# Kernel tuning notes

Hardware: AMD Instinct MI355X
Metric: run time of the kernel (lower is better)

Reference implementation:

```python
import jax, jax.numpy as jnp
import numpy as np

B, N, E = 1024, 4096, 16384
MAX_COL_W, ROW_W = 4, 8


def setup_inputs() -> dict:
    key = jax.random.key(0)
    k1, k2, k3, k4, k5 = jax.random.split(key, 5)
    return {
        "channelLLR": jax.random.normal(k1, (B, N), dtype=jnp.float32),
        "e2oLLR": jax.random.normal(k2, (B, E), dtype=jnp.float32),
        "maxColWeight": MAX_COL_W,
        "edgeToVar": jax.random.randint(k3, (B, N, MAX_COL_W), 0, E, dtype=jnp.int32),
        "edgeToVarMask": jnp.ones((B, N, MAX_COL_W), dtype=jnp.float32),
        "oddToEven": jax.random.randint(k4, (B, E), 0, N, dtype=jnp.int32),
        "edgeToChk": jax.random.randint(k5, (B, E, ROW_W - 1), 0, E, dtype=jnp.int32),
        "rowWeight": ROW_W,
        "alpha": jnp.ones((1,), dtype=jnp.float32),
    }


def reference(channelLLR, e2oLLR, maxColWeight, edgeToVar, edgeToVarMask,
              oddToEven, edgeToChk, rowWeight, alpha):
    b = channelLLR.shape[0]
    # variable-node update: gather incoming edge messages, mask, sum
    msgToVars = jnp.take_along_axis(e2oLLR, edgeToVar.reshape(b, -1), axis=1)
    msgToVars = msgToVars.reshape(b, -1, maxColWeight) * edgeToVarMask  # [B,N,colW]
    llr = channelLLR + jnp.sum(msgToVars, axis=2)                      # [B,N]
    # extrinsic variable-to-check message per edge
    llr = jnp.take_along_axis(llr, oddToEven, axis=1) - e2oLLR         # [B,E]
    # check-node min-sum update over rowWeight-1 peer edges
    msgToChecks = jnp.take_along_axis(llr, edgeToChk.reshape(b, -1), axis=1)
    msgToChecks = msgToChecks.reshape(b, -1, rowWeight - 1)            # [B,E,rowW-1]
    mn = jnp.min(jnp.abs(msgToChecks), axis=2)                         # [B,E]
    sign = jnp.prod(jnp.sign(msgToChecks), axis=2)                     # [B,E]
    e2o = sign * (mn * alpha[0])                                       # [B,E]
    # marginalized posterior LLR per variable node
    out = jnp.take_along_axis(e2o, edgeToVar.reshape(b, -1), axis=1)
    out = out.reshape(b, -1, maxColWeight) * edgeToVarMask
    out = channelLLR + jnp.sum(out, axis=2)                            # [B,N]
    return (out, e2o)
```

## Files before the change

kernel.cpp:

```cpp
#include <hip/hip_runtime.h>

#define BB   1024
#define NN   4096
#define EE   16384
#define COLW 4
#define ROWW1 7
#define TPB  1024
#define NWAVE (TPB / 64)
#define GRP_DW (64 * ROWW1)
#define SCR_DW (NWAVE * GRP_DW)

__global__ __launch_bounds__(TPB) void msl_fused_kernel(
    const float* __restrict__ channelLLR,
    const float* __restrict__ e2oLLR,
    const int*   __restrict__ edgeToVar,
    const float* __restrict__ edgeToVarMask,
    const int*   __restrict__ oddToEven,
    const int*   __restrict__ edgeToChk,
    const float* __restrict__ alpha,
    float*       __restrict__ out,
    float*       __restrict__ e2o_out)
{
    __shared__ __align__(16) float scr_lds[2 * SCR_DW];
    __shared__ __align__(16) float edge_lds[EE];
    const int b    = blockIdx.x;
    const int tid  = threadIdx.x;
    const int wave = tid >> 6;
    const int lane = tid & 63;
    const float alph = alpha[0];

    {
        const float4* __restrict__ src = reinterpret_cast<const float4*>(e2oLLR + (size_t)b * EE);
        float4* dst = reinterpret_cast<float4*>(edge_lds);
        #pragma unroll
        for (int k = 0; k < EE / 4 / TPB; ++k) {
            int i = tid + k * TPB;
            dst[i] = src[i];
        }
    }
    __syncthreads();

    int4   idxreg[NN / TPB];
    float4 mreg[NN / TPB];
    {
        const int4*   __restrict__ ev4 = reinterpret_cast<const int4*>(edgeToVar + (size_t)b * NN * COLW);
        const float4* __restrict__ mk4 = reinterpret_cast<const float4*>(edgeToVarMask + (size_t)b * NN * COLW);
        const float*  __restrict__ chrow = channelLLR + (size_t)b * NN;
        #pragma unroll
        for (int k = 0; k < NN / TPB; ++k) {
            int n = tid + k * TPB;
            int4  idx = ev4[n];
            float4 m  = mk4[n];
            float acc = chrow[n];
            acc += edge_lds[idx.x] * m.x;
            acc += edge_lds[idx.y] * m.y;
            acc += edge_lds[idx.z] * m.z;
            acc += edge_lds[idx.w] * m.w;
            scr_lds[n] = acc;
            idxreg[k] = idx; mreg[k] = m;
        }
    }
    __syncthreads();

    {
        const int* __restrict__ o2erow = oddToEven + (size_t)b * EE;
        #pragma unroll 8
        for (int k = 0; k < EE / TPB; ++k) {
            int e = tid + k * TPB;
            int o = o2erow[e];
            float v = scr_lds[o] - edge_lds[e];
            edge_lds[e] = v;
        }
    }
    __syncthreads();

    float e2oreg[EE / TPB];
    {
        const int* __restrict__ ecrow = edgeToChk + (size_t)b * (size_t)EE * ROWW1;
        float* __restrict__ e2orow = e2o_out + (size_t)b * EE;
        int idx[ROWW1];
        {
            const int* __restrict__ p = ecrow + (size_t)wave * GRP_DW + lane;
            #pragma unroll
            for (int j = 0; j < ROWW1; ++j) idx[j] = p[64 * j];
        }
        #pragma unroll
        for (int it = 0; it < EE / TPB; ++it) {
            const int g = it * NWAVE + wave;
            float* __restrict__ scratch = scr_lds + (it & 1) * SCR_DW + wave * GRP_DW;
            #pragma unroll
            for (int j = 0; j < ROWW1; ++j) scratch[lane + 64 * j] = edge_lds[idx[j]];
            if (it + 1 < EE / TPB) {
                const int* __restrict__ p = ecrow + (size_t)(g + NWAVE) * GRP_DW + lane;
                #pragma unroll
                for (int j = 0; j < ROWW1; ++j) idx[j] = p[64 * j];
            }
            __builtin_amdgcn_wave_barrier();
            asm volatile("s_waitcnt lgkmcnt(0)" ::: "memory");
            __builtin_amdgcn_wave_barrier();
            float mn = 3.0e38f;
            unsigned sgn = 0u;
            const float* __restrict__ sb = scratch + lane * ROWW1;
            #pragma unroll
            for (int j = 0; j < ROWW1; ++j) {
                float u = sb[j];
                sgn ^= __float_as_uint(u);
                mn = fminf(mn, fabsf(u));
            }
            float val = mn * alph;
            float r = __uint_as_float(__float_as_uint(val) ^ (sgn & 0x80000000u));
            e2oreg[it] = r;
            e2orow[64 * g + lane] = r;
        }
    }
    __syncthreads();

    #pragma unroll
    for (int k = 0; k < EE / TPB; ++k) {
        edge_lds[tid + k * TPB] = e2oreg[k];
    }
    __syncthreads();

    {
        float* __restrict__ outrow = out + (size_t)b * NN;
        const float* __restrict__ chrow = channelLLR + (size_t)b * NN;
        #pragma unroll
        for (int k = 0; k < NN / TPB; ++k) {
            int n = tid + k * TPB;
            int4  idx = idxreg[k];
            float4 m  = mreg[k];
            float acc = chrow[n];
            acc += edge_lds[idx.x] * m.x;
            acc += edge_lds[idx.y] * m.y;
            acc += edge_lds[idx.z] * m.z;
            acc += edge_lds[idx.w] * m.w;
            outrow[n] = acc;
        }
    }
}

extern "C" void kernel_launch(void* const* d_in, const int* in_sizes, int n_in,
                              void* d_out, int out_size, void* d_ws, size_t ws_size,
                              hipStream_t stream) {
    const float* channelLLR    = (const float*)d_in[0];
    const float* e2oLLR        = (const float*)d_in[1];
    const int*   edgeToVar     = (const int*)d_in[3];
    const float* edgeToVarMask = (const float*)d_in[4];
    const int*   oddToEven     = (const int*)d_in[5];
    const int*   edgeToChk     = (const int*)d_in[6];
    const float* alpha         = (const float*)d_in[8];

    float* out     = (float*)d_out;
    float* e2o_out = (float*)d_out + (size_t)BB * NN;

    msl_fused_kernel<<<BB, TPB, 0, stream>>>(
        channelLLR, e2oLLR, edgeToVar, edgeToVarMask,
        oddToEven, edgeToChk, alpha, out, e2o_out);
}
```

Before: 166.7 us.

## Make kernel persistent over four rows with double-buffered prefetch of next row

Launches 256 blocks instead of 1024, and each block processes four batch rows in sequence. The next row's e2oLLR is loaded into a second LDS buffer while the current row's check-node loop runs, which is meant to hide global-load latency and cut per-block setup cost. The check-node scratch becomes single-buffered, with an extra waitcnt at the start of each iteration. With 256 blocks on a GPU with 256 CUs this gives one block per CU, so it gives up inter-block latency hiding and load balancing. The larger LDS footprint also limits occupancy.

```diff
diff --git a/kernel.cpp b/kernel.cpp
--- a/kernel.cpp
+++ b/kernel.cpp
@@ -9,6 +9,8 @@
 #define NWAVE (TPB / 64)
 #define GRP_DW (64 * ROWW1)
 #define SCR_DW (NWAVE * GRP_DW)
+#define NBLK 256
+#define RPB  (BB / NBLK)
 
 __global__ __launch_bounds__(TPB) void msl_fused_kernel(
     const float* __restrict__ channelLLR,
@@ -21,41 +23,38 @@
     float*       __restrict__ out,
     float*       __restrict__ e2o_out)
 {
-    __shared__ __align__(16) float scr_lds[2 * SCR_DW];
-    __shared__ __align__(16) float edge_lds[EE];
-    const int b    = blockIdx.x;
+    __shared__ __align__(16) float edge_lds[2][EE];
+    __shared__ __align__(16) float scr_lds[SCR_DW];
     const int tid  = threadIdx.x;
     const int wave = tid >> 6;
     const int lane = tid & 63;
     const float alph = alpha[0];
 
+    int4   idxreg[NN / TPB];
+    float4 mreg[NN / TPB];
+
     {
-        const float4* __restrict__ src = reinterpret_cast<const float4*>(e2oLLR + (size_t)b * EE);
-        float4* dst = reinterpret_cast<float4*>(edge_lds);
+        const float4* __restrict__ src = reinterpret_cast<const float4*>(e2oLLR + (size_t)blockIdx.x * EE);
+        float4* dst = reinterpret_cast<float4*>(&edge_lds[0][0]);
         #pragma unroll
-        for (int k = 0; k < EE / 4 / TPB; ++k) {
-            int i = tid + k * TPB;
-            dst[i] = src[i];
-        }
+        for (int k = 0; k < EE / 4 / TPB; ++k) dst[tid + k * TPB] = src[tid + k * TPB];
     }
     __syncthreads();
 
-    int4   idxreg[NN / TPB];
-    float4 mreg[NN / TPB];
     {
-        const int4*   __restrict__ ev4 = reinterpret_cast<const int4*>(edgeToVar + (size_t)b * NN * COLW);
-        const float4* __restrict__ mk4 = reinterpret_cast<const float4*>(edgeToVarMask + (size_t)b * NN * COLW);
-        const float*  __restrict__ chrow = channelLLR + (size_t)b * NN;
+        const int r = blockIdx.x;
+        const int4*   __restrict__ ev4 = reinterpret_cast<const int4*>(edgeToVar + (size_t)r * NN * COLW);
+        const float4* __restrict__ mk4 = reinterpret_cast<const float4*>(edgeToVarMask + (size_t)r * NN * COLW);
+        const float*  __restrict__ chrow = channelLLR + (size_t)r * NN;
+        const float* buf = &edge_lds[0][0];
         #pragma unroll
         for (int k = 0; k < NN / TPB; ++k) {
             int n = tid + k * TPB;
             int4  idx = ev4[n];
             float4 m  = mk4[n];
             float acc = chrow[n];
-            acc += edge_lds[idx.x] * m.x;
-            acc += edge_lds[idx.y] * m.y;
-            acc += edge_lds[idx.z] * m.z;
-            acc += edge_lds[idx.w] * m.w;
+            acc += buf[idx.x] * m.x; acc += buf[idx.y] * m.y;
+            acc += buf[idx.z] * m.z; acc += buf[idx.w] * m.w;
             scr_lds[n] = acc;
             idxreg[k] = idx; mreg[k] = m;
         }
@@ -63,79 +62,117 @@
     __syncthreads();
 
     {
-        const int* __restrict__ o2erow = oddToEven + (size_t)b * EE;
+        const int* __restrict__ o2erow = oddToEven + (size_t)blockIdx.x * EE;
+        float* buf = &edge_lds[0][0];
         #pragma unroll 8
         for (int k = 0; k < EE / TPB; ++k) {
             int e = tid + k * TPB;
-            int o = o2erow[e];
-            float v = scr_lds[o] - edge_lds[e];
-            edge_lds[e] = v;
+            buf[e] = scr_lds[o2erow[e]] - buf[e];
         }
     }
     __syncthreads();
 
-    float e2oreg[EE / TPB];
-    {
-        const int* __restrict__ ecrow = edgeToChk + (size_t)b * (size_t)EE * ROWW1;
-        float* __restrict__ e2orow = e2o_out + (size_t)b * EE;
-        int idx[ROWW1];
+    for (int i = 0; i < RPB; ++i) {
+        const int r = blockIdx.x + NBLK * i;
+        float* cur = &edge_lds[i & 1][0];
+        float* nxt = &edge_lds[(i + 1) & 1][0];
+        const bool has_next = (i < RPB - 1);
+
+        float e2oreg[EE / TPB];
         {
-            const int* __restrict__ p = ecrow + (size_t)wave * GRP_DW + lane;
-            #pragma unroll
-            for (int j = 0; j < ROWW1; ++j) idx[j] = p[64 * j];
-        }
-        #pragma unroll
-        for (int it = 0; it < EE / TPB; ++it) {
-            const int g = it * NWAVE + wave;
-            float* __restrict__ scratch = scr_lds + (it & 1) * SCR_DW + wave * GRP_DW;
-            #pragma unroll
-            for (int j = 0; j < ROWW1; ++j) scratch[lane + 64 * j] = edge_lds[idx[j]];
-            if (it + 1 < EE / TPB) {
-                const int* __restrict__ p = ecrow + (size_t)(g + NWAVE) * GRP_DW + lane;
+            const int* __restrict__ ecrow = edgeToChk + (size_t)r * (size_t)EE * ROWW1;
+            float* __restrict__ e2orow = e2o_out + (size_t)r * EE;
+            const float4* __restrict__ nsrc = has_next
+                ? reinterpret_cast<const float4*>(e2oLLR + (size_t)(r + NBLK) * EE) : nullptr;
+            float4* ndst = reinterpret_cast<float4*>(nxt);
+            float* __restrict__ scratch = scr_lds + wave * GRP_DW;
+            int idx[ROWW1];
+            {
+                const int* __restrict__ p = ecrow + (size_t)wave * GRP_DW + lane;
                 #pragma unroll
                 for (int j = 0; j < ROWW1; ++j) idx[j] = p[64 * j];
             }
-            __builtin_amdgcn_wave_barrier();
-            asm volatile("s_waitcnt lgkmcnt(0)" ::: "memory");
-            __builtin_amdgcn_wave_barrier();
-            float mn = 3.0e38f;
-            unsigned sgn = 0u;
-            const float* __restrict__ sb = scratch + lane * ROWW1;
+            float4 stage_v;
             #pragma unroll
-            for (int j = 0; j < ROWW1; ++j) {
-                float u = sb[j];
-                sgn ^= __float_as_uint(u);
-                mn = fminf(mn, fabsf(u));
+            for (int it = 0; it < EE / TPB; ++it) {
+                const int g = it * NWAVE + wave;
+                __builtin_amdgcn_wave_barrier();
+                asm volatile("s_waitcnt lgkmcnt(0)" ::: "memory");
+                __builtin_amdgcn_wave_barrier();
+                #pragma unroll
+                for (int j = 0; j < ROWW1; ++j) scratch[lane + 64 * j] = cur[idx[j]];
+                if (has_next) {
+                    if ((it & 3) == 0)      stage_v = nsrc[tid + (it >> 2) * TPB];
+                    else if ((it & 3) == 2) ndst[tid + (it >> 2) * TPB] = stage_v;
+                }
+                if (it + 1 < EE / TPB) {
+                    const int* __restrict__ p = ecrow + (size_t)(g + NWAVE) * GRP_DW + lane;
+                    #pragma unroll
+                    for (int j = 0; j < ROWW1; ++j) idx[j] = p[64 * j];
+                }
+                __builtin_amdgcn_wave_barrier();
+                asm volatile("s_waitcnt lgkmcnt(0)" ::: "memory");
+                __builtin_amdgcn_wave_barrier();
+                float mn = 3.0e38f;
+                unsigned sgn = 0u;
+                const float* __restrict__ sb = scratch + lane * ROWW1;
+                #pragma unroll
+                for (int j = 0; j < ROWW1; ++j) {
+                    float u = sb[j];
+                    sgn ^= __float_as_uint(u);
+                    mn = fminf(mn, fabsf(u));
+                }
+                float val = mn * alph;
+                float rr = __uint_as_float(__float_as_uint(val) ^ (sgn & 0x80000000u));
+                e2oreg[it] = rr;
+                e2orow[64 * g + lane] = rr;
             }
-            float val = mn * alph;
-            float r = __uint_as_float(__float_as_uint(val) ^ (sgn & 0x80000000u));
-            e2oreg[it] = r;
-            e2orow[64 * g + lane] = r;
         }
-    }
-    __syncthreads();
+        __syncthreads();
 
-    #pragma unroll
-    for (int k = 0; k < EE / TPB; ++k) {
-        edge_lds[tid + k * TPB] = e2oreg[k];
-    }
-    __syncthreads();
+        #pragma unroll
+        for (int k = 0; k < EE / TPB; ++k) cur[tid + k * TPB] = e2oreg[k];
+        __syncthreads();
 
-    {
-        float* __restrict__ outrow = out + (size_t)b * NN;
-        const float* __restrict__ chrow = channelLLR + (size_t)b * NN;
-        #pragma unroll
-        for (int k = 0; k < NN / TPB; ++k) {
-            int n = tid + k * TPB;
-            int4  idx = idxreg[k];
-            float4 m  = mreg[k];
-            float acc = chrow[n];
-            acc += edge_lds[idx.x] * m.x;
-            acc += edge_lds[idx.y] * m.y;
-            acc += edge_lds[idx.z] * m.z;
-            acc += edge_lds[idx.w] * m.w;
-            outrow[n] = acc;
+        {
+            const float* __restrict__ chrow = channelLLR + (size_t)r * NN;
+            float* __restrict__ outrow = out + (size_t)r * NN;
+            #pragma unroll
+            for (int k = 0; k < NN / TPB; ++k) {
+                int n = tid + k * TPB;
+                int4  idx = idxreg[k];
+                float4 m  = mreg[k];
+                float acc = chrow[n];
+                acc += cur[idx.x] * m.x; acc += cur[idx.y] * m.y;
+                acc += cur[idx.z] * m.z; acc += cur[idx.w] * m.w;
+                outrow[n] = acc;
+            }
         }
+        if (has_next) {
+            const int rn = r + NBLK;
+            const int4*   __restrict__ ev4 = reinterpret_cast<const int4*>(edgeToVar + (size_t)rn * NN * COLW);
+            const float4* __restrict__ mk4 = reinterpret_cast<const float4*>(edgeToVarMask + (size_t)rn * NN * COLW);
+            const float*  __restrict__ chrow = channelLLR + (size_t)rn * NN;
+            #pragma unroll
+            for (int k = 0; k < NN / TPB; ++k) {
+                int n = tid + k * TPB;
+                int4  idx = ev4[n];
+                float4 m  = mk4[n];
+                float acc = chrow[n];
+                acc += nxt[idx.x] * m.x; acc += nxt[idx.y] * m.y;
+                acc += nxt[idx.z] * m.z; acc += nxt[idx.w] * m.w;
+                scr_lds[n] = acc;
+                idxreg[k] = idx; mreg[k] = m;
+            }
+            __syncthreads();
+            const int* __restrict__ o2erow = oddToEven + (size_t)rn * EE;
+            #pragma unroll 8
+            for (int k = 0; k < EE / TPB; ++k) {
+                int e = tid + k * TPB;
+                nxt[e] = scr_lds[o2erow[e]] - nxt[e];
+            }
+        }
+        __syncthreads();
     }
 }
 
@@ -153,7 +190,7 @@
     float* out     = (float*)d_out;
     float* e2o_out = (float*)d_out + (size_t)BB * NN;
 
-    msl_fused_kernel<<<BB, TPB, 0, stream>>>(
+    msl_fused_kernel<<<NBLK, TPB, 0, stream>>>(
         channelLLR, e2oLLR, edgeToVar, edgeToVarMask,
         oddToEven, edgeToChk, alpha, out, e2o_out);
 }
```

After: 179.4 us. 7.7% more time.

## Halve block size, single-buffer scratch, pack edge indices to raise occupancy

Applied to the files above, without the earlier changes.

Drops the block size from 1024 to 512 threads and adds a min-blocks-per-CU launch bound. The check-node scratch buffer is now single-buffered inside an NN-sized LDS array, so LDS per block shrinks and more blocks can be resident per CU. The edgeToVar indices are stored as packed 16-bit pairs to save registers, since each thread now holds twice as many elements. In exchange, each thread does twice the work per loop, the single-buffered scratch adds a wait before every refill, and the packed indices assume E fits in 16 bits.

```diff
diff --git a/kernel.cpp b/kernel.cpp
--- a/kernel.cpp
+++ b/kernel.cpp
@@ -5,12 +5,12 @@
 #define EE   16384
 #define COLW 4
 #define ROWW1 7
-#define TPB  1024
+#define TPB  512
 #define NWAVE (TPB / 64)
 #define GRP_DW (64 * ROWW1)
-#define SCR_DW (NWAVE * GRP_DW)
+#define NIT  (EE / TPB)
 
-__global__ __launch_bounds__(TPB) void msl_fused_kernel(
+__global__ __launch_bounds__(TPB, 4) void msl_fused_kernel(
     const float* __restrict__ channelLLR,
     const float* __restrict__ e2oLLR,
     const int*   __restrict__ edgeToVar,
@@ -21,7 +21,7 @@
     float*       __restrict__ out,
     float*       __restrict__ e2o_out)
 {
-    __shared__ __align__(16) float scr_lds[2 * SCR_DW];
+    __shared__ __align__(16) float scr_lds[NN];
     __shared__ __align__(16) float edge_lds[EE];
     const int b    = blockIdx.x;
     const int tid  = threadIdx.x;
@@ -40,7 +40,7 @@
     }
     __syncthreads();
 
-    int4   idxreg[NN / TPB];
+    uint2  idxpk[NN / TPB];
     float4 mreg[NN / TPB];
     {
         const int4*   __restrict__ ev4 = reinterpret_cast<const int4*>(edgeToVar + (size_t)b * NN * COLW);
@@ -57,7 +57,9 @@
             acc += edge_lds[idx.z] * m.z;
             acc += edge_lds[idx.w] * m.w;
             scr_lds[n] = acc;
-            idxreg[k] = idx; mreg[k] = m;
+            idxpk[k] = make_uint2((unsigned)idx.x | ((unsigned)idx.y << 16),
+                                  (unsigned)idx.z | ((unsigned)idx.w << 16));
+            mreg[k] = m;
         }
     }
     __syncthreads();
@@ -65,19 +67,18 @@
     {
         const int* __restrict__ o2erow = oddToEven + (size_t)b * EE;
         #pragma unroll 8
-        for (int k = 0; k < EE / TPB; ++k) {
+        for (int k = 0; k < NIT; ++k) {
             int e = tid + k * TPB;
-            int o = o2erow[e];
-            float v = scr_lds[o] - edge_lds[e];
-            edge_lds[e] = v;
+            edge_lds[e] = scr_lds[o2erow[e]] - edge_lds[e];
         }
     }
     __syncthreads();
 
-    float e2oreg[EE / TPB];
+    float e2oreg[NIT];
     {
         const int* __restrict__ ecrow = edgeToChk + (size_t)b * (size_t)EE * ROWW1;
         float* __restrict__ e2orow = e2o_out + (size_t)b * EE;
+        float* __restrict__ scratch = scr_lds + wave * GRP_DW;
         int idx[ROWW1];
         {
             const int* __restrict__ p = ecrow + (size_t)wave * GRP_DW + lane;
@@ -85,12 +86,14 @@
             for (int j = 0; j < ROWW1; ++j) idx[j] = p[64 * j];
         }
         #pragma unroll
-        for (int it = 0; it < EE / TPB; ++it) {
+        for (int it = 0; it < NIT; ++it) {
             const int g = it * NWAVE + wave;
-            float* __restrict__ scratch = scr_lds + (it & 1) * SCR_DW + wave * GRP_DW;
+            __builtin_amdgcn_wave_barrier();
+            asm volatile("s_waitcnt lgkmcnt(0)" ::: "memory");
+            __builtin_amdgcn_wave_barrier();
             #pragma unroll
             for (int j = 0; j < ROWW1; ++j) scratch[lane + 64 * j] = edge_lds[idx[j]];
-            if (it + 1 < EE / TPB) {
+            if (it + 1 < NIT) {
                 const int* __restrict__ p = ecrow + (size_t)(g + NWAVE) * GRP_DW + lane;
                 #pragma unroll
                 for (int j = 0; j < ROWW1; ++j) idx[j] = p[64 * j];
@@ -116,7 +119,7 @@
     __syncthreads();
 
     #pragma unroll
-    for (int k = 0; k < EE / TPB; ++k) {
+    for (int k = 0; k < NIT; ++k) {
         edge_lds[tid + k * TPB] = e2oreg[k];
     }
     __syncthreads();
@@ -127,13 +130,13 @@
         #pragma unroll
         for (int k = 0; k < NN / TPB; ++k) {
             int n = tid + k * TPB;
-            int4  idx = idxreg[k];
+            uint2  pk = idxpk[k];
             float4 m  = mreg[k];
             float acc = chrow[n];
-            acc += edge_lds[idx.x] * m.x;
-            acc += edge_lds[idx.y] * m.y;
-            acc += edge_lds[idx.z] * m.z;
-            acc += edge_lds[idx.w] * m.w;
+            acc += edge_lds[pk.x & 0xFFFFu] * m.x;
+            acc += edge_lds[pk.x >> 16]     * m.y;
+            acc += edge_lds[pk.y & 0xFFFFu] * m.z;
+            acc += edge_lds[pk.y >> 16]     * m.w;
             outrow[n] = acc;
         }
     }
```

After: 180.6 us. 8.4% more time.

## Prefetch indices early, double-buffer check indices, write e2o to separate LDS

Applied to the files above, without the earlier changes.

Loads edgeToVar, mask, channel values and the first two groups of edgeToChk indices into registers before the first barrier, so their global latency overlaps the e2oLLR staging. The check-node loop now prefetches indices two iterations ahead using two alternating register sets, with a single scratch buffer. Results go straight to a new e2o LDS array instead of registers, which removes a barrier and the copy-back pass. The cost is more LDS per block (an extra 64KB) and more registers, which may limit occupancy.

```diff
diff --git a/kernel.cpp b/kernel.cpp
--- a/kernel.cpp
+++ b/kernel.cpp
@@ -9,6 +9,7 @@
 #define NWAVE (TPB / 64)
 #define GRP_DW (64 * ROWW1)
 #define SCR_DW (NWAVE * GRP_DW)
+#define NIT  (EE / TPB)
 
 __global__ __launch_bounds__(TPB) void msl_fused_kernel(
     const float* __restrict__ channelLLR,
@@ -21,13 +22,39 @@
     float*       __restrict__ out,
     float*       __restrict__ e2o_out)
 {
-    __shared__ __align__(16) float scr_lds[2 * SCR_DW];
     __shared__ __align__(16) float edge_lds[EE];
+    __shared__ __align__(16) float e2o_lds[EE];
+    __shared__ __align__(16) float scr_lds[SCR_DW];
     const int b    = blockIdx.x;
     const int tid  = threadIdx.x;
     const int wave = tid >> 6;
     const int lane = tid & 63;
     const float alph = alpha[0];
+
+    const float* __restrict__ chrow = channelLLR + (size_t)b * NN;
+    const int*   __restrict__ ecrow = edgeToChk + (size_t)b * (size_t)EE * ROWW1;
+
+    int4   idxreg[NN / TPB];
+    float4 mreg[NN / TPB];
+    float  chreg[NN / TPB];
+    {
+        const int4*   __restrict__ ev4 = reinterpret_cast<const int4*>(edgeToVar + (size_t)b * NN * COLW);
+        const float4* __restrict__ mk4 = reinterpret_cast<const float4*>(edgeToVarMask + (size_t)b * NN * COLW);
+        #pragma unroll
+        for (int k = 0; k < NN / TPB; ++k) {
+            int n = tid + k * TPB;
+            idxreg[k] = ev4[n];
+            mreg[k]   = mk4[n];
+            chreg[k]  = chrow[n];
+        }
+    }
+    int idxA[ROWW1], idxB[ROWW1];
+    {
+        const int* __restrict__ pA = ecrow + (size_t)wave * GRP_DW + lane;
+        const int* __restrict__ pB = ecrow + (size_t)(NWAVE + wave) * GRP_DW + lane;
+        #pragma unroll
+        for (int j = 0; j < ROWW1; ++j) { idxA[j] = pA[64 * j]; idxB[j] = pB[64 * j]; }
+    }
 
     {
         const float4* __restrict__ src = reinterpret_cast<const float4*>(e2oLLR + (size_t)b * EE);
@@ -40,24 +67,18 @@
     }
     __syncthreads();
 
-    int4   idxreg[NN / TPB];
-    float4 mreg[NN / TPB];
     {
-        const int4*   __restrict__ ev4 = reinterpret_cast<const int4*>(edgeToVar + (size_t)b * NN * COLW);
-        const float4* __restrict__ mk4 = reinterpret_cast<const float4*>(edgeToVarMask + (size_t)b * NN * COLW);
-        const float*  __restrict__ chrow = channelLLR + (size_t)b * NN;
         #pragma unroll
         for (int k = 0; k < NN / TPB; ++k) {
             int n = tid + k * TPB;
-            int4  idx = ev4[n];
-            float4 m  = mk4[n];
-            float acc = chrow[n];
+            int4  idx = idxreg[k];
+            float4 m  = mreg[k];
+            float acc = chreg[k];
             acc += edge_lds[idx.x] * m.x;
             acc += edge_lds[idx.y] * m.y;
             acc += edge_lds[idx.z] * m.z;
             acc += edge_lds[idx.w] * m.w;
             scr_lds[n] = acc;
-            idxreg[k] = idx; mreg[k] = m;
         }
     }
     __syncthreads();
@@ -65,75 +86,74 @@
     {
         const int* __restrict__ o2erow = oddToEven + (size_t)b * EE;
         #pragma unroll 8
-        for (int k = 0; k < EE / TPB; ++k) {
+        for (int k = 0; k < NIT; ++k) {
             int e = tid + k * TPB;
-            int o = o2erow[e];
-            float v = scr_lds[o] - edge_lds[e];
-            edge_lds[e] = v;
+            edge_lds[e] = scr_lds[o2erow[e]] - edge_lds[e];
         }
     }
     __syncthreads();
 
-    float e2oreg[EE / TPB];
     {
-        const int* __restrict__ ecrow = edgeToChk + (size_t)b * (size_t)EE * ROWW1;
-        float* __restrict__ e2orow = e2o_out + (size_t)b * EE;
-        int idx[ROWW1];
-        {
-            const int* __restrict__ p = ecrow + (size_t)wave * GRP_DW + lane;
-            #pragma unroll
-            for (int j = 0; j < ROWW1; ++j) idx[j] = p[64 * j];
+        float* __restrict__ e2orow  = e2o_out + (size_t)b * EE;
+        float* __restrict__ scratch = scr_lds + wave * GRP_DW;
+
+#define P3_ITER(IT, IDX)                                                        \
+        {                                                                       \
+            const int g = (IT) * NWAVE + wave;                                  \
+               \
+            __builtin_amdgcn_wave_barrier();                                    \
+            asm volatile("s_waitcnt lgkmcnt(0)" ::: "memory");                  \
+            __builtin_amdgcn_wave_barrier();                                    \
+            _Pragma("unroll")                                                   \
+            for (int j = 0; j < ROWW1; ++j)                                     \
+                scratch[lane + 64 * j] = edge_lds[IDX[j]];                      \
+            if ((IT) + 2 < NIT) {                                               \
+                const int* __restrict__ p =                                     \
+                    ecrow + (size_t)(g + 2 * NWAVE) * GRP_DW + lane;            \
+                _Pragma("unroll")                                               \
+                for (int j = 0; j < ROWW1; ++j) IDX[j] = p[64 * j];             \
+            }                                                                   \
+                       \
+            __builtin_amdgcn_wave_barrier();                                    \
+            asm volatile("s_waitcnt lgkmcnt(0)" ::: "memory");                  \
+            __builtin_amdgcn_wave_barrier();                                    \
+            float mn = 3.0e38f;                                                 \
+            unsigned sgn = 0u;                                                  \
+            const float* __restrict__ sb = scratch + lane * ROWW1;              \
+            _Pragma("unroll")                                                   \
+            for (int j = 0; j < ROWW1; ++j) {                                   \
+                float u = sb[j];                                                \
+                sgn ^= __float_as_uint(u);                                      \
+                mn = fminf(mn, fabsf(u));                                       \
+            }                                                                   \
+            float val = mn * alph;                                              \
+            float r = __uint_as_float(__float_as_uint(val) ^ (sgn & 0x80000000u)); \
+            e2o_lds[64 * g + lane] = r;                                         \
+            e2orow[64 * g + lane] = r;                                          \
         }
+
         #pragma unroll
-        for (int it = 0; it < EE / TPB; ++it) {
-            const int g = it * NWAVE + wave;
-            float* __restrict__ scratch = scr_lds + (it & 1) * SCR_DW + wave * GRP_DW;
-            #pragma unroll
-            for (int j = 0; j < ROWW1; ++j) scratch[lane + 64 * j] = edge_lds[idx[j]];
-            if (it + 1 < EE / TPB) {
-                const int* __restrict__ p = ecrow + (size_t)(g + NWAVE) * GRP_DW + lane;
-                #pragma unroll
-                for (int j = 0; j < ROWW1; ++j) idx[j] = p[64 * j];
-            }
-            __builtin_amdgcn_wave_barrier();
-            asm volatile("s_waitcnt lgkmcnt(0)" ::: "memory");
-            __builtin_amdgcn_wave_barrier();
-            float mn = 3.0e38f;
-            unsigned sgn = 0u;
-            const float* __restrict__ sb = scratch + lane * ROWW1;
-            #pragma unroll
-            for (int j = 0; j < ROWW1; ++j) {
-                float u = sb[j];
-                sgn ^= __float_as_uint(u);
-                mn = fminf(mn, fabsf(u));
-            }
-            float val = mn * alph;
-            float r = __uint_as_float(__float_as_uint(val) ^ (sgn & 0x80000000u));
-            e2oreg[it] = r;
-            e2orow[64 * g + lane] = r;
+        for (int itp = 0; itp < NIT / 2; ++itp) {
+            P3_ITER(2 * itp,     idxA)
+            P3_ITER(2 * itp + 1, idxB)
         }
+#undef P3_ITER
     }
-    __syncthreads();
 
-    #pragma unroll
-    for (int k = 0; k < EE / TPB; ++k) {
-        edge_lds[tid + k * TPB] = e2oreg[k];
-    }
-    __syncthreads();
+    asm volatile("s_waitcnt lgkmcnt(0)\n\ts_barrier" ::: "memory");
 
     {
         float* __restrict__ outrow = out + (size_t)b * NN;
-        const float* __restrict__ chrow = channelLLR + (size_t)b * NN;
         #pragma unroll
         for (int k = 0; k < NN / TPB; ++k) {
             int n = tid + k * TPB;
             int4  idx = idxreg[k];
             float4 m  = mreg[k];
-            float acc = chrow[n];
-            acc += edge_lds[idx.x] * m.x;
-            acc += edge_lds[idx.y] * m.y;
-            acc += edge_lds[idx.z] * m.z;
-            acc += edge_lds[idx.w] * m.w;
+            float acc = chreg[k];
+            acc += e2o_lds[idx.x] * m.x;
+            acc += e2o_lds[idx.y] * m.y;
+            acc += e2o_lds[idx.z] * m.z;
+            acc += e2o_lds[idx.w] * m.w;
             outrow[n] = acc;
         }
     }
```

Result: slower. 170.4 us (+2.2%).
